# Optimization experiments

Measured on AMD Instinct MI355X. Metric: run time of the kernel, lower is better.

The kernel has to match this reference:

```python
import jax, jax.numpy as jnp
import numpy as np

K_FRAC = 0.5  # init arg k (keep fraction)


def setup_inputs() -> dict:
    key = jax.random.key(0)
    k1, k2, k3, k4, k5 = jax.random.split(key, 5)
    B, N, F = 1, 100000, 128
    E, Fe = 1600000, 32
    x = jax.random.normal(k1, (B, N, F), jnp.float32)
    edge_index = jax.random.randint(k2, (2, E), 0, N, dtype=jnp.int32)
    edge_attr = jax.random.normal(k3, (B, E, Fe), jnp.float32)
    # nn.Linear(in_dim, 1) params
    proj_w = jax.random.normal(k4, (1, F), jnp.float32) / jnp.sqrt(F)
    proj_b = jax.random.normal(k5, (1,), jnp.float32) * 0.01
    return {"x": x, "edge_attr": edge_attr, "proj_w": proj_w,
            "proj_b": proj_b, "edge_index": edge_index}


def reference(x, edge_attr, proj_w, proj_b, edge_index):
    B, N, F = x.shape
    # linear score + sigmoid (dropout p=0 -> identity)
    scores = jax.nn.sigmoid(jnp.einsum('bnf,of->bno', x, proj_w)[..., 0] + proj_b[0])  # [B,N]
    # torch.kthvalue(scores, kth, dim=1): kth smallest (1-indexed)
    kth = int((1.0 - K_FRAC) * N)
    kth_scores = jnp.sort(scores, axis=1)[:, kth - 1:kth]  # [B,1]
    mask = scores >= kth_scores  # [B,N]
    n_keep = int(N * K_FRAC)
    # stable descending sort of mask.float() -> true indices first, in original order
    pool_indices = jnp.argsort(jnp.where(mask, 0, 1), axis=1)[:, :n_keep]  # [B,n_keep]
    new_x = jnp.take_along_axis(x, pool_indices[..., None], axis=1)  # [B,n_keep,F]
    # 1-D node mask shared across batch (as in the torch code)
    node_mask = jnp.zeros((N,), bool).at[pool_indices].set(True)
    pool_edges = node_mask[edge_index[0]] & node_mask[edge_index[1]]  # [E] bool
    new_edge_index = edge_index[:, pool_edges]        # [2, E'] (data-dependent, eager)
    new_edge_attr = edge_attr[:, pool_edges]          # [B, E', Fe]
    mapping = jnp.full((N,), -1, jnp.int32).at[pool_indices].set(
        jnp.broadcast_to(jnp.arange(n_keep, dtype=jnp.int32), pool_indices.shape))
    new_edge_index_ordered = mapping[new_edge_index]
    return (new_x, new_edge_index, new_edge_index_ordered, new_edge_attr,
            pool_indices, pool_edges)
```

## Files before the change

### kernel.cpp

```cpp
#include <hip/hip_runtime.h>
#include <math.h>

__global__ __launch_bounds__(256) void scores_kernel(
    const float* __restrict__ x, const float* __restrict__ w,
    const float* __restrict__ bptr, int N, int F, unsigned* __restrict__ scores) {
  int node = blockIdx.x * 4 + (threadIdx.x >> 6);
  int lane = threadIdx.x & 63;
  if (node >= N) return;
  const float* xr = x + (size_t)node * F;
  double acc = 0.0;
  for (int f = lane; f < F; f += 64)
    acc += (double)xr[f] * (double)w[f];
  for (int off = 32; off > 0; off >>= 1)
    acc += __shfl_down(acc, off, 64);
  if (lane == 0) {
    double z = acc + (double)bptr[0];
    double s = 1.0 / (1.0 + exp(-z));
    scores[node] = __float_as_uint((float)s);
  }
}

__global__ __launch_bounds__(256) void hist_kernel(
    const unsigned* __restrict__ scores, int N, unsigned* __restrict__ hist,
    const unsigned* __restrict__ sel, int pass) {
  int i = blockIdx.x * 256 + threadIdx.x;
  if (i >= N) return;
  unsigned bits = scores[i];
  if (pass == 0) {
    atomicAdd(&hist[bits >> 16], 1u);
  } else {
    if ((bits >> 16) == sel[0]) atomicAdd(&hist[bits & 0xFFFFu], 1u);
  }
}

__global__ __launch_bounds__(256) void select_kernel(
    const unsigned* __restrict__ hist, const unsigned* __restrict__ qptr, unsigned qconst,
    unsigned* __restrict__ outB, unsigned* __restrict__ outRem) {
  __shared__ unsigned tot[256];
  __shared__ unsigned bins[256];
  __shared__ unsigned sChunk, sRem;
  int t = threadIdx.x;
  unsigned q = qptr ? *qptr : qconst;
  const unsigned* hp = hist + t * 256;
  unsigned s = 0;
  for (int j = 0; j < 256; j++) s += hp[j];
  tot[t] = s;
  __syncthreads();
  if (t == 0) {
    unsigned cum = 0; int c = 0;
    for (; c < 256; c++) { if (q < cum + tot[c]) break; cum += tot[c]; }
    sChunk = (unsigned)c; sRem = q - cum;
  }
  __syncthreads();
  bins[t] = hist[sChunk * 256 + t];
  __syncthreads();
  if (t == 0) {
    unsigned cum = 0; unsigned q2 = sRem; int bi = 0;
    for (; bi < 256; bi++) { if (q2 < cum + bins[bi]) break; cum += bins[bi]; }
    *outB = sChunk * 256 + bi;
    *outRem = q2 - cum;
  }
}

__global__ __launch_bounds__(256) void node_mask_sums(
    const unsigned* __restrict__ scores, const unsigned* __restrict__ sel, int N,
    unsigned* __restrict__ sums) {
  int i = blockIdx.x * 256 + threadIdx.x;
  unsigned T = (sel[0] << 16) | sel[2];
  int m = (i < N) && (scores[i] >= T);
  unsigned long long bal = __ballot(m);
  __shared__ unsigned wv[4];
  int lane = threadIdx.x & 63, wave = threadIdx.x >> 6;
  if (lane == 0) wv[wave] = (unsigned)__popcll(bal);
  __syncthreads();
  if (threadIdx.x == 0) sums[blockIdx.x] = wv[0] + wv[1] + wv[2] + wv[3];
}

__global__ __launch_bounds__(256) void scan_exclusive(unsigned* __restrict__ data, int n) {
  __shared__ unsigned tmp[256];
  __shared__ unsigned carry;
  int t = threadIdx.x;
  if (t == 0) carry = 0;
  __syncthreads();
  for (int base = 0; base < n; base += 256) {
    int i = base + t;
    unsigned v = (i < n) ? data[i] : 0;
    tmp[t] = v;
    __syncthreads();
    for (int s = 1; s < 256; s <<= 1) {
      unsigned a = (t >= s) ? tmp[t - s] : 0;
      __syncthreads();
      tmp[t] += a;
      __syncthreads();
    }
    unsigned incl = tmp[t];
    unsigned c = carry;
    if (i < n) data[i] = c + incl - v;
    unsigned total = tmp[255];
    __syncthreads();
    if (t == 0) carry = c + total;
    __syncthreads();
  }
}

__global__ __launch_bounds__(256) void node_finalize(
    const unsigned* __restrict__ scores, const unsigned* __restrict__ sel,
    const unsigned* __restrict__ sums_ex, int N, int n_keep,
    int* __restrict__ map, int* __restrict__ poolsrc, float* __restrict__ out_pool) {
  int i = blockIdx.x * 256 + threadIdx.x;
  unsigned T = (sel[0] << 16) | sel[2];
  int m = (i < N) && (scores[i] >= T);
  unsigned long long bal = __ballot(m);
  int lane = threadIdx.x & 63, wave = threadIdx.x >> 6;
  __shared__ unsigned wv[4];
  if (lane == 0) wv[wave] = (unsigned)__popcll(bal);
  __syncthreads();
  unsigned pre = 0;
  for (int k = 0; k < wave; k++) pre += wv[k];
  pre += (unsigned)__popcll(bal & ((1ull << lane) - 1ull));
  if (i < N) {
    int mv = -1;
    if (m) {
      unsigned rank = sums_ex[blockIdx.x] + pre;
      if (rank < (unsigned)n_keep) {
        mv = (int)rank;
        poolsrc[rank] = i;
        out_pool[rank] = (float)i;
      }
    }
    map[i] = mv;
  }
}

__global__ __launch_bounds__(256) void gather_x(
    const float* __restrict__ x, const int* __restrict__ poolsrc, int n_keep, int F, int N,
    float* __restrict__ outx) {
  int r = blockIdx.x * 4 + (threadIdx.x >> 6);
  int lane = threadIdx.x & 63;
  if (r >= n_keep) return;
  int src = poolsrc[r];
  src = src < 0 ? 0 : (src >= N ? N - 1 : src);
  const float2* s = (const float2*)(x + (size_t)src * F);
  float2* d = (float2*)(outx + (size_t)r * F);
  int half = F / 2;
  for (int j = lane; j < half; j += 64) d[j] = s[j];
}

__global__ __launch_bounds__(256) void edge_mask_sums(
    const int* __restrict__ ei, const int* __restrict__ map, int E,
    float* __restrict__ out_pe, unsigned* __restrict__ sums) {
  int e = blockIdx.x * 256 + threadIdx.x;
  int m = 0;
  if (e < E) {
    int a = ei[e], b = ei[E + e];
    m = (map[a] >= 0) && (map[b] >= 0);
    out_pe[e] = m ? 1.0f : 0.0f;
  }
  unsigned long long bal = __ballot(m);
  __shared__ unsigned wv[4];
  int lane = threadIdx.x & 63, wave = threadIdx.x >> 6;
  if (lane == 0) wv[wave] = (unsigned)__popcll(bal);
  __syncthreads();
  if (threadIdx.x == 0) sums[blockIdx.x] = wv[0] + wv[1] + wv[2] + wv[3];
}

__global__ __launch_bounds__(256) void edge_finalize(
    const int* __restrict__ ei, const int* __restrict__ map,
    const unsigned* __restrict__ sums_ex, int E, int Ek, int Fe,
    const float* __restrict__ attr, float* __restrict__ out,
    size_t o_ei, size_t o_eio, size_t o_attr) {
  int e = blockIdx.x * 256 + threadIdx.x;
  int m = 0, a = 0, b = 0, ma = -1, mb = -1;
  if (e < E) {
    a = ei[e]; b = ei[E + e];
    ma = map[a]; mb = map[b];
    m = (ma >= 0) && (mb >= 0);
  }
  unsigned long long bal = __ballot(m);
  int lane = threadIdx.x & 63, wave = threadIdx.x >> 6;
  __shared__ unsigned wv[4];
  if (lane == 0) wv[wave] = (unsigned)__popcll(bal);
  __syncthreads();
  unsigned pre = 0;
  for (int k = 0; k < wave; k++) pre += wv[k];
  pre += (unsigned)__popcll(bal & ((1ull << lane) - 1ull));
  if (m) {
    unsigned p = sums_ex[blockIdx.x] + pre;
    out[o_ei + p]              = (float)a;
    out[o_ei + (size_t)Ek + p] = (float)b;
    out[o_eio + p]              = (float)ma;
    out[o_eio + (size_t)Ek + p] = (float)mb;
    float4* dst = (float4*)(out + o_attr + (size_t)p * Fe);
    const float4* src = (const float4*)(attr + (size_t)e * Fe);
    for (int j = 0; j < Fe / 4; j++) dst[j] = src[j];
  }
}

extern "C" void kernel_launch(void* const* d_in, const int* in_sizes, int n_in,
                              void* d_out, int out_size, void* d_ws, size_t ws_size,
                              hipStream_t stream) {
  const int F  = in_sizes[2];
  const int E  = in_sizes[4] / 2;
  const int N  = in_sizes[0] / F;
  const int Fe = in_sizes[1] / E;
  const int n_keep = N / 2;
  const unsigned q = (unsigned)(N - n_keep - 1);
  const int Ek = (int)(((long long)out_size - (long long)n_keep * F - n_keep - E) / (4 + Fe));

  const float* x    = (const float*)d_in[0];
  const float* attr = (const float*)d_in[1];
  const float* w    = (const float*)d_in[2];
  const float* b    = (const float*)d_in[3];
  const int*   ei   = (const int*)d_in[4];
  float*       out  = (float*)d_out;

  const size_t o_newx = 0;
  const size_t o_ei   = (size_t)n_keep * F;
  const size_t o_eio  = o_ei + 2 * (size_t)Ek;
  const size_t o_attr = o_eio + 2 * (size_t)Ek;
  const size_t o_pool = o_attr + (size_t)Ek * Fe;
  const size_t o_pe   = o_pool + (size_t)n_keep;

  char* wsb = (char*)d_ws;
  size_t off = 0;
  auto carve = [&](size_t bytes) -> void* {
    void* p = wsb + off;
    off = (off + bytes + 255) & ~(size_t)255;
    return p;
  };
  const int nb_n = (N + 255) / 256;
  const int nb_e = (E + 255) / 256;
  unsigned* scores = (unsigned*)carve((size_t)N * 4);
  unsigned* hist1  = (unsigned*)carve((size_t)65536 * 4);
  unsigned* hist2  = (unsigned*)carve((size_t)65536 * 4);
  unsigned* sel    = (unsigned*)carve(64);
  unsigned* nsum   = (unsigned*)carve((size_t)nb_n * 4);
  unsigned* esum   = (unsigned*)carve((size_t)nb_e * 4);
  int* map         = (int*)carve((size_t)N * 4);
  int* poolsrc     = (int*)carve((size_t)n_keep * 4);

  hipMemsetAsync(hist1, 0, (size_t)2 * 65536 * 4, stream);
  scores_kernel<<<(N + 3) / 4, 256, 0, stream>>>(x, w, b, N, F, scores);
  hist_kernel<<<nb_n, 256, 0, stream>>>(scores, N, hist1, sel, 0);
  select_kernel<<<1, 256, 0, stream>>>(hist1, nullptr, q, sel + 0, sel + 1);
  hist_kernel<<<nb_n, 256, 0, stream>>>(scores, N, hist2, sel, 1);
  select_kernel<<<1, 256, 0, stream>>>(hist2, sel + 1, 0u, sel + 2, sel + 3);
  node_mask_sums<<<nb_n, 256, 0, stream>>>(scores, sel, N, nsum);
  scan_exclusive<<<1, 256, 0, stream>>>(nsum, nb_n);
  node_finalize<<<nb_n, 256, 0, stream>>>(scores, sel, nsum, N, n_keep, map, poolsrc, out + o_pool);
  gather_x<<<(n_keep + 3) / 4, 256, 0, stream>>>(x, poolsrc, n_keep, F, N, out + o_newx);
  edge_mask_sums<<<nb_e, 256, 0, stream>>>(ei, map, E, out + o_pe, esum);
  scan_exclusive<<<1, 256, 0, stream>>>(esum, nb_e);
  edge_finalize<<<nb_e, 256, 0, stream>>>(ei, map, esum, E, Ek, Fe, attr,
                                          out, o_ei, o_eio, o_attr);
}
```

Baseline: 543.0 us.

## Fuse compaction passes with decoupled look-back scan and merge histogram into scoring

```diff
diff --git a/kernel.cpp b/kernel.cpp
--- a/kernel.cpp
+++ b/kernel.cpp
@@ -1,36 +1,73 @@
 #include <hip/hip_runtime.h>
 #include <math.h>
 
+#define DEVINL __device__ __forceinline__
+
+DEVINL unsigned lookback_base(unsigned long long* look, int id, unsigned total, int lane) {
+  if (id == 0) {
+    if (lane == 0)
+      __hip_atomic_store(&look[0], (2ull << 40) | (unsigned long long)total,
+                         __ATOMIC_RELEASE, __HIP_MEMORY_SCOPE_AGENT);
+    return 0;
+  }
+  if (lane == 0)
+    __hip_atomic_store(&look[id], (1ull << 40) | (unsigned long long)total,
+                       __ATOMIC_RELEASE, __HIP_MEMORY_SCOPE_AGENT);
+  unsigned base = 0;
+  int p = id - 1;
+  for (;;) {
+    int idx = p - lane;
+    unsigned long long v = 0;
+    if (idx >= 0) {
+      do {
+        v = __hip_atomic_load(&look[idx], __ATOMIC_ACQUIRE, __HIP_MEMORY_SCOPE_AGENT);
+        if ((v >> 40) == 0) __builtin_amdgcn_s_sleep(1);
+      } while ((v >> 40) == 0);
+    }
+    unsigned long long m2 = __ballot((idx >= 0) && ((v >> 40) == 2));
+    int stop = m2 ? (__ffsll(m2) - 1) : 64;
+    unsigned c = ((idx >= 0) && (lane <= stop)) ? (unsigned)(v & 0xFFFFFFFFull) : 0u;
+    for (int off = 32; off > 0; off >>= 1) c += __shfl_down(c, off, 64);
+    if (lane == 0) base += c;
+    if (m2) break;
+    p -= 64;
+  }
+  if (lane == 0)
+    __hip_atomic_store(&look[id], (2ull << 40) | (unsigned long long)(base + total),
+                       __ATOMIC_RELEASE, __HIP_MEMORY_SCOPE_AGENT);
+  return base;
+}
+
 __global__ __launch_bounds__(256) void scores_kernel(
     const float* __restrict__ x, const float* __restrict__ w,
-    const float* __restrict__ bptr, int N, int F, unsigned* __restrict__ scores) {
+    const float* __restrict__ bptr, int N, int F,
+    unsigned* __restrict__ scores, unsigned* __restrict__ hist0) {
   int node = blockIdx.x * 4 + (threadIdx.x >> 6);
   int lane = threadIdx.x & 63;
   if (node >= N) return;
-  const float* xr = x + (size_t)node * F;
+  const float2* xr = (const float2*)(x + (size_t)node * F);
+  const float2* w2 = (const float2*)w;
   double acc = 0.0;
-  for (int f = lane; f < F; f += 64)
-    acc += (double)xr[f] * (double)w[f];
-  for (int off = 32; off > 0; off >>= 1)
-    acc += __shfl_down(acc, off, 64);
+  for (int f = lane; f < F / 2; f += 64) {
+    float2 xv = xr[f], wv = w2[f];
+    acc += (double)xv.x * (double)wv.x + (double)xv.y * (double)wv.y;
+  }
+  for (int off = 32; off > 0; off >>= 1) acc += __shfl_down(acc, off, 64);
   if (lane == 0) {
     double z = acc + (double)bptr[0];
-    double s = 1.0 / (1.0 + exp(-z));
-    scores[node] = __float_as_uint((float)s);
-  }
-}
-
-__global__ __launch_bounds__(256) void hist_kernel(
+    unsigned bits = __float_as_uint((float)(1.0 / (1.0 + exp(-z))));
+    scores[node] = bits;
+    atomicAdd(&hist0[bits >> 16], 1u);
+  }
+}
+
+__global__ __launch_bounds__(256) void hist1_kernel(
     const unsigned* __restrict__ scores, int N, unsigned* __restrict__ hist,
-    const unsigned* __restrict__ sel, int pass) {
+    const unsigned* __restrict__ sel) {
   int i = blockIdx.x * 256 + threadIdx.x;
   if (i >= N) return;
   unsigned bits = scores[i];
-  if (pass == 0) {
-    atomicAdd(&hist[bits >> 16], 1u);
-  } else {
-    if ((bits >> 16) == sel[0]) atomicAdd(&hist[bits & 0xFFFFu], 1u);
-  }
+  if ((bits >> 16) == sel[0]) atomicAdd(&hist[bits & 0xFFFFu], 1u);
 }
 
 __global__ __launch_bounds__(256) void select_kernel(
@@ -62,137 +99,115 @@
   }
 }
 
-__global__ __launch_bounds__(256) void node_mask_sums(
-    const unsigned* __restrict__ scores, const unsigned* __restrict__ sel, int N,
-    unsigned* __restrict__ sums) {
-  int i = blockIdx.x * 256 + threadIdx.x;
+__global__ __launch_bounds__(256) void node_pass(
+    const unsigned* __restrict__ scores, const unsigned* __restrict__ sel,
+    const float* __restrict__ x, int N, int F, int n_keep,
+    unsigned* __restrict__ ctr, unsigned long long* __restrict__ look,
+    int* __restrict__ map, float* __restrict__ out_pool, float* __restrict__ out_x) {
+  __shared__ unsigned s_id, s_base;
+  __shared__ unsigned wv[4];
+  __shared__ int keep_src[256];
+  int t = threadIdx.x;
+  if (t == 0) s_id = atomicAdd(ctr, 1u);
+  __syncthreads();
+  int id = (int)s_id;
+  int i = id * 256 + t;
   unsigned T = (sel[0] << 16) | sel[2];
   int m = (i < N) && (scores[i] >= T);
   unsigned long long bal = __ballot(m);
+  int lane = t & 63, wave = t >> 6;
+  if (lane == 0) wv[wave] = (unsigned)__popcll(bal);
+  __syncthreads();
+  unsigned total = wv[0] + wv[1] + wv[2] + wv[3];
+  unsigned pre = (unsigned)__popcll(bal & ((1ull << lane) - 1ull));
+  for (int k = 0; k < wave; k++) pre += wv[k];
+  if (t < 64) {
+    unsigned b = lookback_base(look, id, total, lane);
+    if (lane == 0) s_base = b;
+  }
+  __syncthreads();
+  unsigned base = s_base;
+  int kc = n_keep - (int)base;
+  kc = kc < 0 ? 0 : (kc > (int)total ? (int)total : kc);
+  if (i < N) {
+    int rank = -1;
+    if (m && base + pre < (unsigned)n_keep) {
+      rank = (int)(base + pre);
+      out_pool[rank] = (float)i;
+      keep_src[pre] = i;
+    }
+    map[i] = rank;
+  }
+  __syncthreads();
+  int tpr = F / 4;
+  int rpi = 256 / tpr;
+  int jrow = t / tpr, c = t % tpr;
+  for (int j0 = 0; j0 < kc; j0 += rpi) {
+    int j = j0 + jrow;
+    if (j < kc) {
+      const float4* s = (const float4*)(x + (size_t)keep_src[j] * F);
+      float4* d = (float4*)(out_x + (size_t)(base + (unsigned)j) * F);
+      d[c] = s[c];
+    }
+  }
+}
+
+__global__ __launch_bounds__(256) void edge_pass(
+    const int* __restrict__ ei, const int* __restrict__ map,
+    const float* __restrict__ attr, int E, int Ek, int Fe,
+    unsigned* __restrict__ ctr, unsigned long long* __restrict__ look,
+    float* __restrict__ out, size_t o_ei, size_t o_eio, size_t o_attr, size_t o_pe) {
+  __shared__ unsigned s_id, s_base;
   __shared__ unsigned wv[4];
-  int lane = threadIdx.x & 63, wave = threadIdx.x >> 6;
-  if (lane == 0) wv[wave] = (unsigned)__popcll(bal);
-  __syncthreads();
-  if (threadIdx.x == 0) sums[blockIdx.x] = wv[0] + wv[1] + wv[2] + wv[3];
-}
-
-__global__ __launch_bounds__(256) void scan_exclusive(unsigned* __restrict__ data, int n) {
-  __shared__ unsigned tmp[256];
-  __shared__ unsigned carry;
+  __shared__ int keepE[256];
+  __shared__ float kA[256], kB[256], kMA[256], kMB[256];
   int t = threadIdx.x;
-  if (t == 0) carry = 0;
-  __syncthreads();
-  for (int base = 0; base < n; base += 256) {
-    int i = base + t;
-    unsigned v = (i < n) ? data[i] : 0;
-    tmp[t] = v;
-    __syncthreads();
-    for (int s = 1; s < 256; s <<= 1) {
-      unsigned a = (t >= s) ? tmp[t - s] : 0;
-      __syncthreads();
-      tmp[t] += a;
-      __syncthreads();
-    }
-    unsigned incl = tmp[t];
-    unsigned c = carry;
-    if (i < n) data[i] = c + incl - v;
-    unsigned total = tmp[255];
-    __syncthreads();
-    if (t == 0) carry = c + total;
-    __syncthreads();
-  }
-}
-
-__global__ __launch_bounds__(256) void node_finalize(
-    const unsigned* __restrict__ scores, const unsigned* __restrict__ sel,
-    const unsigned* __restrict__ sums_ex, int N, int n_keep,
-    int* __restrict__ map, int* __restrict__ poolsrc, float* __restrict__ out_pool) {
-  int i = blockIdx.x * 256 + threadIdx.x;
-  unsigned T = (sel[0] << 16) | sel[2];
-  int m = (i < N) && (scores[i] >= T);
-  unsigned long long bal = __ballot(m);
-  int lane = threadIdx.x & 63, wave = threadIdx.x >> 6;
-  __shared__ unsigned wv[4];
-  if (lane == 0) wv[wave] = (unsigned)__popcll(bal);
-  __syncthreads();
-  unsigned pre = 0;
-  for (int k = 0; k < wave; k++) pre += wv[k];
-  pre += (unsigned)__popcll(bal & ((1ull << lane) - 1ull));
-  if (i < N) {
-    int mv = -1;
-    if (m) {
-      unsigned rank = sums_ex[blockIdx.x] + pre;
-      if (rank < (unsigned)n_keep) {
-        mv = (int)rank;
-        poolsrc[rank] = i;
-        out_pool[rank] = (float)i;
-      }
-    }
-    map[i] = mv;
-  }
-}
-
-__global__ __launch_bounds__(256) void gather_x(
-    const float* __restrict__ x, const int* __restrict__ poolsrc, int n_keep, int F, int N,
-    float* __restrict__ outx) {
-  int r = blockIdx.x * 4 + (threadIdx.x >> 6);
-  int lane = threadIdx.x & 63;
-  if (r >= n_keep) return;
-  int src = poolsrc[r];
-  src = src < 0 ? 0 : (src >= N ? N - 1 : src);
-  const float2* s = (const float2*)(x + (size_t)src * F);
-  float2* d = (float2*)(outx + (size_t)r * F);
-  int half = F / 2;
-  for (int j = lane; j < half; j += 64) d[j] = s[j];
-}
-
-__global__ __launch_bounds__(256) void edge_mask_sums(
-    const int* __restrict__ ei, const int* __restrict__ map, int E,
-    float* __restrict__ out_pe, unsigned* __restrict__ sums) {
-  int e = blockIdx.x * 256 + threadIdx.x;
-  int m = 0;
-  if (e < E) {
-    int a = ei[e], b = ei[E + e];
-    m = (map[a] >= 0) && (map[b] >= 0);
-    out_pe[e] = m ? 1.0f : 0.0f;
-  }
-  unsigned long long bal = __ballot(m);
-  __shared__ unsigned wv[4];
-  int lane = threadIdx.x & 63, wave = threadIdx.x >> 6;
-  if (lane == 0) wv[wave] = (unsigned)__popcll(bal);
-  __syncthreads();
-  if (threadIdx.x == 0) sums[blockIdx.x] = wv[0] + wv[1] + wv[2] + wv[3];
-}
-
-__global__ __launch_bounds__(256) void edge_finalize(
-    const int* __restrict__ ei, const int* __restrict__ map,
-    const unsigned* __restrict__ sums_ex, int E, int Ek, int Fe,
-    const float* __restrict__ attr, float* __restrict__ out,
-    size_t o_ei, size_t o_eio, size_t o_attr) {
-  int e = blockIdx.x * 256 + threadIdx.x;
+  if (t == 0) s_id = atomicAdd(ctr, 1u);
+  __syncthreads();
+  int id = (int)s_id;
+  int e = id * 256 + t;
   int m = 0, a = 0, b = 0, ma = -1, mb = -1;
   if (e < E) {
     a = ei[e]; b = ei[E + e];
     ma = map[a]; mb = map[b];
     m = (ma >= 0) && (mb >= 0);
+    out[o_pe + e] = m ? 1.0f : 0.0f;
   }
   unsigned long long bal = __ballot(m);
-  int lane = threadIdx.x & 63, wave = threadIdx.x >> 6;
-  __shared__ unsigned wv[4];
+  int lane = t & 63, wave = t >> 6;
   if (lane == 0) wv[wave] = (unsigned)__popcll(bal);
   __syncthreads();
-  unsigned pre = 0;
+  unsigned total = wv[0] + wv[1] + wv[2] + wv[3];
+  unsigned pre = (unsigned)__popcll(bal & ((1ull << lane) - 1ull));
   for (int k = 0; k < wave; k++) pre += wv[k];
-  pre += (unsigned)__popcll(bal & ((1ull << lane) - 1ull));
   if (m) {
-    unsigned p = sums_ex[blockIdx.x] + pre;
-    out[o_ei + p]              = (float)a;
-    out[o_ei + (size_t)Ek + p] = (float)b;
-    out[o_eio + p]              = (float)ma;
-    out[o_eio + (size_t)Ek + p] = (float)mb;
-    float4* dst = (float4*)(out + o_attr + (size_t)p * Fe);
-    const float4* src = (const float4*)(attr + (size_t)e * Fe);
-    for (int j = 0; j < Fe / 4; j++) dst[j] = src[j];
+    keepE[pre] = e;
+    kA[pre] = (float)a; kB[pre] = (float)b;
+    kMA[pre] = (float)ma; kMB[pre] = (float)mb;
+  }
+  if (t < 64) {
+    unsigned bs = lookback_base(look, id, total, lane);
+    if (lane == 0) s_base = bs;
+  }
+  __syncthreads();
+  unsigned base = s_base;
+  for (unsigned j = t; j < total; j += 256) {
+    unsigned p = base + j;
+    out[o_ei + p]               = kA[j];
+    out[o_ei + (size_t)Ek + p]  = kB[j];
+    out[o_eio + p]              = kMA[j];
+    out[o_eio + (size_t)Ek + p] = kMB[j];
+  }
+  int tpr = Fe / 4;
+  int rpi = 256 / tpr;
+  int jrow = t / tpr, c = t % tpr;
+  for (int j0 = 0; j0 < (int)total; j0 += rpi) {
+    int j = j0 + jrow;
+    if (j < (int)total) {
+      const float4* s = (const float4*)(attr + (size_t)keepE[j] * Fe);
+      float4* d = (float4*)(out + o_attr + (size_t)(base + (unsigned)j) * Fe);
+      d[c] = s[c];
+    }
   }
 }
 
@@ -214,12 +229,14 @@
   const int*   ei   = (const int*)d_in[4];
   float*       out  = (float*)d_out;
 
-  const size_t o_newx = 0;
   const size_t o_ei   = (size_t)n_keep * F;
   const size_t o_eio  = o_ei + 2 * (size_t)Ek;
   const size_t o_attr = o_eio + 2 * (size_t)Ek;
   const size_t o_pool = o_attr + (size_t)Ek * Fe;
   const size_t o_pe   = o_pool + (size_t)n_keep;
+
+  const int nb_n = (N + 255) / 256;
+  const int nb_e = (E + 255) / 256;
 
   char* wsb = (char*)d_ws;
   size_t off = 0;
@@ -228,29 +245,23 @@
     off = (off + bytes + 255) & ~(size_t)255;
     return p;
   };
-  const int nb_n = (N + 255) / 256;
-  const int nb_e = (E + 255) / 256;
+  unsigned* hist0 = (unsigned*)carve((size_t)65536 * 4);
+  unsigned* hist1 = (unsigned*)carve((size_t)65536 * 4);
+  unsigned* sel   = (unsigned*)carve(64);
+  unsigned* ctrs  = (unsigned*)carve(64);
+  unsigned long long* lookN = (unsigned long long*)carve((size_t)nb_n * 8);
+  unsigned long long* lookE = (unsigned long long*)carve((size_t)nb_e * 8);
+  const size_t zero_bytes = off;
   unsigned* scores = (unsigned*)carve((size_t)N * 4);
-  unsigned* hist1  = (unsigned*)carve((size_t)65536 * 4);
-  unsigned* hist2  = (unsigned*)carve((size_t)65536 * 4);
-  unsigned* sel    = (unsigned*)carve(64);
-  unsigned* nsum   = (unsigned*)carve((size_t)nb_n * 4);
-  unsigned* esum   = (unsigned*)carve((size_t)nb_e * 4);
   int* map         = (int*)carve((size_t)N * 4);
-  int* poolsrc     = (int*)carve((size_t)n_keep * 4);
-
-  hipMemsetAsync(hist1, 0, (size_t)2 * 65536 * 4, stream);
-  scores_kernel<<<(N + 3) / 4, 256, 0, stream>>>(x, w, b, N, F, scores);
-  hist_kernel<<<nb_n, 256, 0, stream>>>(scores, N, hist1, sel, 0);
-  select_kernel<<<1, 256, 0, stream>>>(hist1, nullptr, q, sel + 0, sel + 1);
-  hist_kernel<<<nb_n, 256, 0, stream>>>(scores, N, hist2, sel, 1);
-  select_kernel<<<1, 256, 0, stream>>>(hist2, sel + 1, 0u, sel + 2, sel + 3);
-  node_mask_sums<<<nb_n, 256, 0, stream>>>(scores, sel, N, nsum);
-  scan_exclusive<<<1, 256, 0, stream>>>(nsum, nb_n);
-  node_finalize<<<nb_n, 256, 0, stream>>>(scores, sel, nsum, N, n_keep, map, poolsrc, out + o_pool);
-  gather_x<<<(n_keep + 3) / 4, 256, 0, stream>>>(x, poolsrc, n_keep, F, N, out + o_newx);
-  edge_mask_sums<<<nb_e, 256, 0, stream>>>(ei, map, E, out + o_pe, esum);
-  scan_exclusive<<<1, 256, 0, stream>>>(esum, nb_e);
-  edge_finalize<<<nb_e, 256, 0, stream>>>(ei, map, esum, E, Ek, Fe, attr,
-                                          out, o_ei, o_eio, o_attr);
-}
+
+  hipMemsetAsync(wsb, 0, zero_bytes, stream);
+  scores_kernel<<<(N + 3) / 4, 256, 0, stream>>>(x, w, b, N, F, scores, hist0);
+  select_kernel<<<1, 256, 0, stream>>>(hist0, nullptr, q, sel + 0, sel + 1);
+  hist1_kernel<<<nb_n, 256, 0, stream>>>(scores, N, hist1, sel);
+  select_kernel<<<1, 256, 0, stream>>>(hist1, sel + 1, 0u, sel + 2, sel + 3);
+  node_pass<<<nb_n, 256, 0, stream>>>(scores, sel, x, N, F, n_keep,
+                                      ctrs + 0, lookN, map, out + o_pool, out);
+  edge_pass<<<nb_e, 256, 0, stream>>>(ei, map, attr, E, Ek, Fe,
+                                      ctrs + 8, lookE, out, o_ei, o_eio, o_attr, o_pe);
+}
```

New measurement: 1.249 ms. 130% more time.
